# Kernel tuning notes

Measured on AMD Instinct MI355X. Metric: run time of the kernel, lower is better.

## Reference

```python
import jax, jax.numpy as jnp
import numpy as np

B, CIN, COUT, L, K, D = 64, 128, 256, 1024, 3, 2
P = (K - 1) * D  # causal padding = 4
THRESH = 0.1
SLOPE = 0.2  # LeakyReLU negative slope


def setup_inputs() -> dict:
    key = jax.random.key(0)
    ks = jax.random.split(key, 24)
    rn = lambda k, shape, s=0.05: jax.random.normal(k, shape, dtype=jnp.float32) * s
    return {
        "x": rn(ks[0], (B, CIN, L), 1.0),
        "conv1_w": rn(ks[1], (COUT, CIN, K)),
        "conv1_b": rn(ks[2], (COUT,)),
        "Wz_w": rn(ks[3], (COUT, COUT)), "Wz_b": rn(ks[4], (COUT,)),
        "Uz_w": rn(ks[5], (COUT, COUT)), "Uz_b": rn(ks[6], (COUT,)),
        "Wr_w": rn(ks[7], (COUT, COUT)), "Wr_b": rn(ks[8], (COUT,)),
        "Ur_w": rn(ks[9], (COUT, COUT)), "Ur_b": rn(ks[10], (COUT,)),
        "Wh_w": rn(ks[11], (COUT, COUT)), "Wh_b": rn(ks[12], (COUT,)),
        "Uh_w": rn(ks[13], (COUT, COUT)), "Uh_b": rn(ks[14], (COUT,)),
        "conv2_w": rn(ks[15], (COUT, COUT, K)),
        "conv2_b": rn(ks[16], (COUT,)),
        "skip_w": rn(ks[17], (COUT, CIN, 1)),
        "skip_b": rn(ks[18], (COUT,)),
        "aw": jnp.ones((1,), jnp.float32),  # AttentionZeroedLayer param, init ones
    }


def _causal_conv(x, w, b):
    # x: [B,C,L], w: [O,I,K]; pad both sides by P then chomp the right tail
    y = jax.lax.conv_general_dilated(
        x, w, window_strides=(1,), padding=[(P, P)], rhs_dilation=(D,),
        dimension_numbers=("NCH", "OIH", "NCH"))
    y = y + b[None, :, None]
    return y[:, :, :-P] if P > 0 else y


def reference(x, conv1_w, conv1_b, Wz_w, Wz_b, Uz_w, Uz_b, Wr_w, Wr_b,
              Ur_w, Ur_b, Wh_w, Wh_b, Uh_w, Uh_b, conv2_w, conv2_b,
              skip_w, skip_b, aw):
    res = x
    # conv1 -> chomp -> LeakyReLU (dropout=0, identity in eval)
    h1 = jax.nn.leaky_relu(_causal_conv(x, conv1_w, conv1_b), SLOPE)  # [B,COUT,L]
    xt = h1.transpose(0, 2, 1)  # [B,L,C]
    # precompute input-side GRU projections as batched GEMMs
    xz = jnp.einsum("blc,hc->blh", xt, Wz_w) + Wz_b
    xr = jnp.einsum("blc,hc->blh", xt, Wr_w) + Wr_b
    xh = jnp.einsum("blc,hc->blh", xt, Wh_w) + Wh_b

    def step(h, ins):
        xz_t, xr_t, xh_t = ins
        z = jax.nn.sigmoid(xz_t + h @ Uz_w.T + Uz_b)
        r = jax.nn.sigmoid(xr_t + h @ Ur_w.T + Ur_b)
        h_tilde = jnp.tanh(xh_t + r * (h @ Uh_w.T + Uh_b))
        h_new = (1 - z) * h + z * h_tilde
        return h_new, h_new

    h0 = jnp.zeros((B, COUT), x.dtype)
    _, hs = jax.lax.scan(step, h0, (xz.transpose(1, 0, 2),
                                    xr.transpose(1, 0, 2),
                                    xh.transpose(1, 0, 2)))  # [L,B,C]
    g = hs.transpose(1, 2, 0)  # [B,COUT,L]
    # AttentionZeroedLayer: zero elements with |g| < threshold * sigmoid(aw)
    gate = jax.nn.sigmoid(aw)[0]
    g = jnp.where(jnp.abs(g) < THRESH * gate, jnp.zeros_like(g), g)
    # conv2 -> chomp -> LeakyReLU
    y = jax.nn.leaky_relu(_causal_conv(g, conv2_w, conv2_b), SLOPE)
    # 1x1 skip connection (in_channels != out_channels)
    res = jax.lax.conv_general_dilated(
        res, skip_w, window_strides=(1,), padding=[(0, 0)],
        dimension_numbers=("NCH", "OIH", "NCH")) + skip_b[None, :, None]
    return y + res
```

## Files before the change

### kernel.cpp

```cpp
#include <hip/hip_runtime.h>
#include <hip/hip_bf16.h>


typedef _Float16 f16;
typedef _Float16 h2_t __attribute__((ext_vector_type(2)));

__device__ __forceinline__ float bf1(unsigned short s){ return __uint_as_float(((unsigned)s)<<16); }

__device__ __forceinline__ unsigned packh2(float a, float b){
  h2_t h; h[0] = (f16)a; h[1] = (f16)b;
  return *(unsigned*)&h;
}
__device__ __forceinline__ unsigned bf2h2(unsigned u){
  return packh2(bf1((unsigned short)(u & 0xffffu)), bf1((unsigned short)(u >> 16)));
}

__device__ __forceinline__ float fdot2(unsigned a, unsigned b, float c){
#if __has_builtin(__builtin_amdgcn_fdot2)
  return __builtin_amdgcn_fdot2(*(h2_t*)&a, *(h2_t*)&b, c, false);
#else
  h2_t x = *(h2_t*)&a, y = *(h2_t*)&b;
  return c + (float)x[0]*(float)y[0] + (float)x[1]*(float)y[1];
#endif
}

__device__ __forceinline__ unsigned short f2bf(float f){
  __hip_bfloat16 h = __float2bfloat16(f);
  return *(unsigned short*)&h;
}
__device__ __forceinline__ unsigned packbf2(float a, float b){
  return (unsigned)f2bf(a) | ((unsigned)f2bf(b)<<16);
}
__device__ __forceinline__ float h2lo(unsigned u){ h2_t h = *(h2_t*)&u; return (float)h[0]; }
__device__ __forceinline__ float h2hi(unsigned u){ h2_t h = *(h2_t*)&u; return (float)h[1]; }

__device__ __forceinline__ bool aw_is_f32(const void* aw){
  return ((const unsigned*)aw)[0] == 0x3F800000u;
}

__device__ __forceinline__ float dpp_add_b1(float v){
  int x = __builtin_amdgcn_update_dpp(0, __float_as_int(v), 0xB1, 0xF, 0xF, true);
  return v + __int_as_float(x);
}
__device__ __forceinline__ float dpp_add_4e(float v){
  int x = __builtin_amdgcn_update_dpp(0, __float_as_int(v), 0x4E, 0xF, 0xF, true);
  return v + __int_as_float(x);
}
__device__ __forceinline__ float red4(float v){
  return dpp_add_4e(dpp_add_b1(v));
}

__global__ void k_repack(const void* __restrict__ w1,  const void* __restrict__ w2,
                         const void* __restrict__ Wz,  const void* __restrict__ Wr,
                         const void* __restrict__ Wh,  const void* __restrict__ wsk,
                         const void* __restrict__ Uz,  const void* __restrict__ Ur,
                         const void* __restrict__ Uh,
                         const void* __restrict__ b1,  const void* __restrict__ Wzb,
                         const void* __restrict__ Wrb, const void* __restrict__ Whb,
                         const void* __restrict__ Uzb, const void* __restrict__ Urb,
                         const void* __restrict__ Uhb, const void* __restrict__ b2,
                         const void* __restrict__ bsk, const void* __restrict__ aw,
                         f16* __restrict__ p1, f16* __restrict__ p2,
                         f16* __restrict__ pz, f16* __restrict__ pr,
                         f16* __restrict__ ph, f16* __restrict__ ps,
                         f16* __restrict__ puz, f16* __restrict__ pur,
                         f16* __restrict__ puh, float* __restrict__ bc)
{
  const bool f32 = aw_is_f32(aw);
  auto G = [&](const void* p, int idx)->float{
    return f32 ? ((const float*)p)[idx] : bf1(((const unsigned short*)p)[idx]);
  };
  int i = blockIdx.x*256 + threadIdx.x;
  if (i < 196608){
    int t=i/65536, r=i%65536, cc=r>>11, r2=r&2047, o=r2>>3, ci=r2&7, c=cc*8+ci;
    p2[i] = (f16)G(w2, o*768 + c*3 + t);
  }
  if (i < 98304){
    int t=i/32768, r=i%32768, cc=r>>11, r2=r&2047, o=r2>>3, ci=r2&7, c=cc*8+ci;
    p1[i] = (f16)G(w1, o*384 + c*3 + t);
  }
  if (i < 65536){
    int cc=i>>11, r2=i&2047, o=r2>>3, ci=r2&7, c=cc*8+ci;
    int s = o*256 + c;
    pz[i]=(f16)G(Wz, s); pr[i]=(f16)G(Wr, s); ph[i]=(f16)G(Wh, s);
    puz[i]=(f16)G(Uz, i); pur[i]=(f16)G(Ur, i); puh[i]=(f16)G(Uh, i);
  }
  if (i < 32768){
    int cc=i>>11, r2=i&2047, o=r2>>3, ci=r2&7, c=cc*8+ci;
    ps[i]=(f16)G(wsk, o*128 + c);
  }
  if (i < 2304){
    int which = i>>8, j = i&255;
    const void* src[9] = {b1, Wzb, Wrb, Whb, Uzb, Urb, Uhb, b2, bsk};
    bc[i] = G(src[which], j);
  }
  if (i == 2304){
    float v = G(aw, 0);
    bc[2304] = 0.1f / (1.f + __expf(-v));
    bc[2305] = f32 ? 1.f : 0.f;
  }
}

__global__ __launch_bounds__(256,2) void k_conv1proj(
    const void* __restrict__ x,
    const f16* __restrict__ W1,
    const f16* __restrict__ WZ, const f16* __restrict__ WR, const f16* __restrict__ WH,
    const float* __restrict__ bc,
    f16* __restrict__ XZ, f16* __restrict__ XR, f16* __restrict__ XH,
    int Lc, int t0)
{
  __shared__ unsigned smem_u[12544];
  f16* xa = (f16*)smem_u;
  unsigned* tileA = smem_u + 4352;
  f16* hy = (f16*)(smem_u + 4352);
  const int b = blockIdx.y;
  const int lt = blockIdx.x*64;
  const int gl0 = t0 + lt;
  const int tid = threadIdx.x, lb = tid&7, ob = tid>>3;
  const bool f32 = (bc[2305] != 0.f);

  #pragma unroll
  for (int k=0;k<17;k++){
    int idx = tid + k*256;
    int c = idx/34, lp = idx - c*34;
    int gl = gl0 - 4 + lp*2;
    unsigned u = 0u;
    if (gl >= 0){
      if (f32){
        float2 v = *(const float2*)((const float*)x + ((size_t)b*128 + c)*1024 + gl);
        u = packh2(v.x, v.y);
      } else {
        u = bf2h2(*(const unsigned*)((const unsigned short*)x + ((size_t)b*128 + c)*1024 + gl));
      }
    }
    tileA[c*35 + lp] = u;
  }
  __syncthreads();
  #pragma unroll
  for (int k=0;k<17;k++){
    int idx = tid + k*256;
    int row = idx>>6, cp = idx&63;
    unsigned u0 = tileA[(2*cp)*35 + (row>>1)];
    unsigned u1 = tileA[(2*cp+1)*35 + (row>>1)];
    unsigned short s0 = (row&1)? (unsigned short)(u0>>16):(unsigned short)(u0&0xffffu);
    unsigned short s1 = (row&1)? (unsigned short)(u1>>16):(unsigned short)(u1&0xffffu);
    int sw = (cp>>2) ^ ((row>>3)&7);
    *(unsigned*)(&xa[row*128 + sw*8 + (cp&3)*2]) = (unsigned)s0 | ((unsigned)s1<<16);
  }
  __syncthreads();

  float acc[8][8];
  uint4 wreg[8], wnext[8];

  #pragma unroll
  for (int i=0;i<8;i++)
    #pragma unroll
    for (int j=0;j<8;j++) acc[i][j]=0.f;
  #pragma unroll
  for (int oi=0;oi<8;oi++) wreg[oi] = *(const uint4*)(W1 + ob*64 + oi*8);
  for (int ch=0; ch<48; ch++){
    if (ch+1 < 48){
      const f16* wn = W1 + (size_t)(ch+1)*2048 + ob*64;
      #pragma unroll
      for (int oi=0;oi<8;oi++) wnext[oi] = *(const uint4*)(wn + oi*8);
    }
    int t = ch>>4, cc = ch&15;
    #pragma unroll
    for (int li=0; li<8; li++){
      int row = lb*8 + li + t*2;
      int sw = cc ^ ((row>>3)&7);
      uint4 a = *(const uint4*)(&xa[row*128 + sw*8]);
      #pragma unroll
      for (int oi=0; oi<8; oi++){
        acc[li][oi] = fdot2(a.x, wreg[oi].x, acc[li][oi]);
        acc[li][oi] = fdot2(a.y, wreg[oi].y, acc[li][oi]);
        acc[li][oi] = fdot2(a.z, wreg[oi].z, acc[li][oi]);
        acc[li][oi] = fdot2(a.w, wreg[oi].w, acc[li][oi]);
      }
    }
    #pragma unroll
    for (int oi=0;oi<8;oi++) wreg[oi] = wnext[oi];
  }
  {
    const float* bp = bc + 0 + ob*8;
    #pragma unroll
    for (int li=0; li<8; li++){
      int row = lb*8 + li;
      f16 vals[8];
      #pragma unroll
      for (int oi=0;oi<8;oi++){
        float v = acc[li][oi] + bp[oi];
        vals[oi] = (f16)((v>0.f) ? v : 0.2f*v);
      }
      *(uint4*)(&hy[row*256 + ((ob ^ ((row>>3)&7))<<3)]) = *(uint4*)vals;
    }
  }
  __syncthreads();

  const f16* Wg[3] = {WZ, WR, WH};
  f16* Og[3] = {XZ, XR, XH};
  for (int g3=0; g3<3; g3++){
    const f16* Wp = Wg[g3];
    #pragma unroll
    for (int i=0;i<8;i++)
      #pragma unroll
      for (int j=0;j<8;j++) acc[i][j]=0.f;
    #pragma unroll
    for (int oi=0;oi<8;oi++) wreg[oi] = *(const uint4*)(Wp + ob*64 + oi*8);
    for (int ch=0; ch<32; ch++){
      if (ch+1 < 32){
        const f16* wn = Wp + (size_t)(ch+1)*2048 + ob*64;
        #pragma unroll
        for (int oi=0;oi<8;oi++) wnext[oi] = *(const uint4*)(wn + oi*8);
      }
      #pragma unroll
      for (int li=0; li<8; li++){
        int row = lb*8 + li;
        int sw = ch ^ ((row>>3)&7);
        uint4 a = *(const uint4*)(&hy[row*256 + sw*8]);
        #pragma unroll
        for (int oi=0; oi<8; oi++){
          acc[li][oi] = fdot2(a.x, wreg[oi].x, acc[li][oi]);
          acc[li][oi] = fdot2(a.y, wreg[oi].y, acc[li][oi]);
          acc[li][oi] = fdot2(a.z, wreg[oi].z, acc[li][oi]);
          acc[li][oi] = fdot2(a.w, wreg[oi].w, acc[li][oi]);
        }
      }
      #pragma unroll
      for (int oi=0;oi<8;oi++) wreg[oi] = wnext[oi];
    }
    f16* Ob = Og[g3] + ((size_t)b*Lc + lt)*256 + ob*8;
    #pragma unroll
    for (int li=0; li<8; li++){
      f16 vals[8];
      #pragma unroll
      for (int oi=0;oi<8;oi++){
        int o = ob*8 + oi;
        float bias = bc[256 + g3*256 + o] + ((g3<2) ? bc[1024 + g3*256 + o] : 0.f);
        vals[oi] = (f16)(acc[li][oi] + bias);
      }
      *(uint4*)(Ob + (size_t)(lb*8 + li)*256) = *(uint4*)vals;
    }
  }
}

__global__ __launch_bounds__(512, 1)
void k_scan(
    const f16* __restrict__ XZ, const f16* __restrict__ XR, const f16* __restrict__ XH,
    const f16* __restrict__ pUz, const f16* __restrict__ pUr, const f16* __restrict__ pUh,
    const float* __restrict__ bc,
    f16* __restrict__ G, float* __restrict__ carry,
    int Lc, int first)
{
  const int b = blockIdx.x, tid = threadIdx.x;
  const int kp = tid&3, grp = tid>>2, r0 = grp*2;
  __shared__ unsigned hb[2][160];

  {
    f16* gb = G + (size_t)b*(Lc+4)*256;
    int row = tid>>7, col = tid&127;
    unsigned v = 0u;
    if (!first) v = *(unsigned*)(gb + (size_t)(Lc+row)*256 + col*2);
    *(unsigned*)(gb + (size_t)row*256 + col*2) = v;
  }

  unsigned uz0[32],uz1[32],ur0[32],ur1[32],uh0[32],uh1[32];
  const int cbase = kp*64;
  #pragma unroll
  for (int j4=0;j4<8;j4++){
    uint4 q;
    q = *(const uint4*)(pUz + r0*256     + cbase + j4*8);
    uz0[j4*4+0]=q.x; uz0[j4*4+1]=q.y; uz0[j4*4+2]=q.z; uz0[j4*4+3]=q.w;
    q = *(const uint4*)(pUz + (r0+1)*256 + cbase + j4*8);
    uz1[j4*4+0]=q.x; uz1[j4*4+1]=q.y; uz1[j4*4+2]=q.z; uz1[j4*4+3]=q.w;
    q = *(const uint4*)(pUr + r0*256     + cbase + j4*8);
    ur0[j4*4+0]=q.x; ur0[j4*4+1]=q.y; ur0[j4*4+2]=q.z; ur0[j4*4+3]=q.w;
    q = *(const uint4*)(pUr + (r0+1)*256 + cbase + j4*8);
    ur1[j4*4+0]=q.x; ur1[j4*4+1]=q.y; ur1[j4*4+2]=q.z; ur1[j4*4+3]=q.w;
    q = *(const uint4*)(pUh + r0*256     + cbase + j4*8);
    uh0[j4*4+0]=q.x; uh0[j4*4+1]=q.y; uh0[j4*4+2]=q.z; uh0[j4*4+3]=q.w;
    q = *(const uint4*)(pUh + (r0+1)*256 + cbase + j4*8);
    uh1[j4*4+0]=q.x; uh1[j4*4+1]=q.y; uh1[j4*4+2]=q.z; uh1[j4*4+3]=q.w;
  }
  #pragma unroll
  for (int j=0;j<32;j++){
    asm volatile("" : "+v"(uz0[j]), "+v"(uz1[j]), "+v"(ur0[j]));
    asm volatile("" : "+v"(ur1[j]), "+v"(uh0[j]), "+v"(uh1[j]));
  }
  const float bh0=bc[1536+r0], bh1=bc[1536+r0+1];
  const float thr = bc[2304];
  float hp0, hp1;
  if (first){ hp0 = 0.f; hp1 = 0.f; }
  else { hp0 = carry[b*256 + r0]; hp1 = carry[b*256 + r0 + 1]; }
  const int wslot = (grp>>5)*40 + (grp&31);
  if (kp == 0) hb[0][wslot] = packh2(hp0, hp1);

  const f16* xzp = XZ + (size_t)b*Lc*256 + r0;
  const f16* xrp = XR + (size_t)b*Lc*256 + r0;
  const f16* xhp = XH + (size_t)b*Lc*256 + r0;
  f16* gp = G + (size_t)b*(Lc+4)*256 + r0;

  unsigned xzv = *(const unsigned*)(xzp);
  unsigned xrv = *(const unsigned*)(xrp);
  unsigned xhv = *(const unsigned*)(xhp);
  __syncthreads();

  for (int t=0; t<Lc; t++){
    const int tn = (t+1 < Lc) ? t+1 : t;
    const unsigned nz = *(const unsigned*)(xzp + (size_t)tn*256);
    const unsigned nr = *(const unsigned*)(xrp + (size_t)tn*256);
    const unsigned nh = *(const unsigned*)(xhp + (size_t)tn*256);

    const unsigned* hbr = hb[t&1] + kp*40;
    float az0=0,az1=0,ar0=0,ar1=0,ah0=0,ah1=0;
    #pragma unroll
    for (int j4=0;j4<8;j4++){
      const uint4 hv = *(const uint4*)(hbr + j4*4);
      const unsigned hw[4] = {hv.x, hv.y, hv.z, hv.w};
      #pragma unroll
      for (int p=0;p<4;p++){
        const int J = j4*4+p;
        az0 = fdot2(hw[p], uz0[J], az0);
        az1 = fdot2(hw[p], uz1[J], az1);
        ar0 = fdot2(hw[p], ur0[J], ar0);
        ar1 = fdot2(hw[p], ur1[J], ar1);
        ah0 = fdot2(hw[p], uh0[J], ah0);
        ah1 = fdot2(hw[p], uh1[J], ah1);
      }
    }
    az0 = red4(az0); az1 = red4(az1);
    ar0 = red4(ar0); ar1 = red4(ar1);
    ah0 = red4(ah0); ah1 = red4(ah1);

    const float z0  = 1.f/(1.f+__expf(-(h2lo(xzv)+az0)));
    const float z1  = 1.f/(1.f+__expf(-(h2hi(xzv)+az1)));
    const float rr0 = 1.f/(1.f+__expf(-(h2lo(xrv)+ar0)));
    const float rr1 = 1.f/(1.f+__expf(-(h2hi(xrv)+ar1)));
    const float e0  = __expf(2.f*(h2lo(xhv)+rr0*(ah0+bh0)));
    const float e1  = __expf(2.f*(h2hi(xhv)+rr1*(ah1+bh1)));
    const float hh0 = 1.f - 2.f/(e0+1.f);
    const float hh1 = 1.f - 2.f/(e1+1.f);
    const float hn0 = (1.f-z0)*hp0 + z0*hh0;
    const float hn1 = (1.f-z1)*hp1 + z1*hh1;
    hp0 = hn0; hp1 = hn1;
    if (kp == 0){
      const float g0 = (fabsf(hn0) < thr) ? 0.f : hn0;
      const float g1 = (fabsf(hn1) < thr) ? 0.f : hn1;
      *(unsigned*)(gp + (size_t)(t+4)*256) = packh2(g0, g1);
      hb[(t+1)&1][wslot] = packh2(hn0, hn1);
    }
    xzv = nz; xrv = nr; xhv = nh;
    __syncthreads();
  }
  if (kp == 0){
    carry[b*256 + r0]     = hp0;
    carry[b*256 + r0 + 1] = hp1;
  }
}

__global__ __launch_bounds__(256,2) void k_final(const f16* __restrict__ G,
    const void* __restrict__ x, const f16* __restrict__ W2,
    const f16* __restrict__ WS, const float* __restrict__ bc,
    void* __restrict__ out, int Lc, int t0)
{
  __shared__ unsigned smem2[8704];
  f16* atG = (f16*)smem2;
  const int b = blockIdx.y;
  const int lt = blockIdx.x*64;
  const int gl0 = t0 + lt;
  const int tid = threadIdx.x, lb = tid&7, ob = tid>>3;
  const bool f32 = (bc[2305] != 0.f);

  {
    const f16* Ab = G + (size_t)b*(Lc+4)*256 + (size_t)lt*256;
    for (int idx=tid; idx<68*32; idx+=256){
      int row = idx>>5, cc = idx&31;
      uint4 v = *(const uint4*)(Ab + (size_t)row*256 + cc*8);
      *(uint4*)(&atG[row*256 + ((cc ^ ((row>>3)&7))<<3)]) = v;
    }
  }
  __syncthreads();

  float acc[8][8];
  #pragma unroll
  for (int i=0;i<8;i++)
    #pragma unroll
    for (int j=0;j<8;j++) acc[i][j]=0.f;

  uint4 wreg[8], wnext[8];
  #pragma unroll
  for (int oi=0;oi<8;oi++) wreg[oi] = *(const uint4*)(W2 + ob*64 + oi*8);
  for (int ch=0; ch<96; ch++){
    if (ch+1 < 96){
      const f16* wn = W2 + (size_t)(ch+1)*2048 + ob*64;
      #pragma unroll
      for (int oi=0;oi<8;oi++) wnext[oi] = *(const uint4*)(wn + oi*8);
    }
    int t = ch>>5, cc = ch&31;
    #pragma unroll
    for (int li=0; li<8; li++){
      int row = lb*8 + li + t*2;
      uint4 a = *(const uint4*)(&atG[row*256 + ((cc ^ ((row>>3)&7))<<3)]);
      #pragma unroll
      for (int oi=0; oi<8; oi++){
        acc[li][oi] = fdot2(a.x, wreg[oi].x, acc[li][oi]);
        acc[li][oi] = fdot2(a.y, wreg[oi].y, acc[li][oi]);
        acc[li][oi] = fdot2(a.z, wreg[oi].z, acc[li][oi]);
        acc[li][oi] = fdot2(a.w, wreg[oi].w, acc[li][oi]);
      }
    }
    #pragma unroll
    for (int oi=0;oi<8;oi++) wreg[oi] = wnext[oi];
  }
  {
    const float* bp = bc + 1792 + ob*8;
    #pragma unroll
    for (int li=0;li<8;li++)
      #pragma unroll
      for (int oi=0;oi<8;oi++){
        float v = acc[li][oi] + bp[oi];
        acc[li][oi] = (v>0.f) ? v : 0.2f*v;
      }
  }
  __syncthreads();

  unsigned* tileB = smem2;
  f16* xa2 = (f16*)(smem2 + 4352);
  #pragma unroll
  for (int k=0;k<16;k++){
    int idx = tid + k*256;
    int c = idx>>5, lp = idx&31;
    unsigned u;
    if (f32){
      float2 v = *(const float2*)((const float*)x + ((size_t)b*128 + c)*1024 + gl0 + lp*2);
      u = packh2(v.x, v.y);
    } else {
      u = bf2h2(*(const unsigned*)((const unsigned short*)x + ((size_t)b*128 + c)*1024 + gl0 + lp*2));
    }
    tileB[c*33 + lp] = u;
  }
  __syncthreads();
  #pragma unroll
  for (int k=0;k<16;k++){
    int idx = tid + k*256;
    int row = idx>>6, cp = idx&63;
    unsigned u0 = tileB[(2*cp)*33 + (row>>1)];
    unsigned u1 = tileB[(2*cp+1)*33 + (row>>1)];
    unsigned short s0 = (row&1)? (unsigned short)(u0>>16):(unsigned short)(u0&0xffffu);
    unsigned short s1 = (row&1)? (unsigned short)(u1>>16):(unsigned short)(u1&0xffffu);
    int sw = (cp>>2) ^ ((row>>3)&7);
    *(unsigned*)(&xa2[row*128 + sw*8 + (cp&3)*2]) = (unsigned)s0 | ((unsigned)s1<<16);
  }
  __syncthreads();

  #pragma unroll
  for (int oi=0;oi<8;oi++) wreg[oi] = *(const uint4*)(WS + ob*64 + oi*8);
  for (int ch=0; ch<16; ch++){
    if (ch+1 < 16){
      const f16* wn = WS + (size_t)(ch+1)*2048 + ob*64;
      #pragma unroll
      for (int oi=0;oi<8;oi++) wnext[oi] = *(const uint4*)(wn + oi*8);
    }
    #pragma unroll
    for (int li=0; li<8; li++){
      int row = lb*8 + li;
      int sw = ch ^ ((row>>3)&7);
      uint4 a = *(const uint4*)(&xa2[row*128 + sw*8]);
      #pragma unroll
      for (int oi=0; oi<8; oi++){
        acc[li][oi] = fdot2(a.x, wreg[oi].x, acc[li][oi]);
        acc[li][oi] = fdot2(a.y, wreg[oi].y, acc[li][oi]);
        acc[li][oi] = fdot2(a.z, wreg[oi].z, acc[li][oi]);
        acc[li][oi] = fdot2(a.w, wreg[oi].w, acc[li][oi]);
      }
    }
    #pragma unroll
    for (int oi=0;oi<8;oi++) wreg[oi] = wnext[oi];
  }
  {
    const float* sp = bc + 2048 + ob*8;
    #pragma unroll
    for (int oi=0;oi<8;oi++){
      int o = ob*8 + oi;
      size_t base = ((size_t)b*256 + o)*1024 + gl0 + lb*8;
      if (f32){
        float st[8];
        #pragma unroll
        for (int j=0;j<8;j++) st[j] = acc[j][oi] + sp[oi];
        *(uint4*)((float*)out + base)     = *(uint4*)&st[0];
        *(uint4*)((float*)out + base + 4) = *(uint4*)&st[4];
      } else {
        unsigned st[4];
        #pragma unroll
        for (int j=0;j<4;j++)
          st[j] = packbf2(acc[2*j][oi] + sp[oi], acc[2*j+1][oi] + sp[oi]);
        *(uint4*)((unsigned short*)out + base) = *(uint4*)st;
      }
    }
  }
}

extern "C" void kernel_launch(void* const* d_in, const int* in_sizes, int n_in,
                              void* d_out, int out_size, void* d_ws, size_t ws_size,
                              hipStream_t stream)
{
  const void* x   = d_in[0];
  const void* w1  = d_in[1];
  const void* b1  = d_in[2];
  const void* Wz  = d_in[3];
  const void* Wzb = d_in[4];
  const void* Uz  = d_in[5];
  const void* Uzb = d_in[6];
  const void* Wr  = d_in[7];
  const void* Wrb = d_in[8];
  const void* Ur  = d_in[9];
  const void* Urb = d_in[10];
  const void* Wh  = d_in[11];
  const void* Whb = d_in[12];
  const void* Uh  = d_in[13];
  const void* Uhb = d_in[14];
  const void* w2  = d_in[15];
  const void* b2  = d_in[16];
  const void* wsk = d_in[17];
  const void* bsk = d_in[18];
  const void* aw  = d_in[19];

  auto need = [](long long Lc)->size_t{
    return (size_t)(2LL*(758784LL + 3LL*64*Lc*256 + 64LL*(Lc+4)*256));
  };
  int Lc = 1024;
  if (ws_size < need(1024)) Lc = 256;
  if (ws_size < need(256))  Lc = 64;
  const int NCH = 1024 / Lc;

  f16* W = (f16*)d_ws;
  f16*   w1p   = W;
  f16*   w2p   = W + 98304;
  f16*   wzp   = W + 294912;
  f16*   wrp   = W + 360448;
  f16*   whp   = W + 425984;
  f16*   wsp   = W + 491520;
  f16*   uzp   = W + 524288;
  f16*   urp   = W + 589824;
  f16*   uhp   = W + 655360;
  float* bc    = (float*)(W + 720896);
  float* carry = (float*)(W + 726016);
  f16*   xz    = W + 758784;
  f16*   xr    = xz + (size_t)64*Lc*256;
  f16*   xh    = xr + (size_t)64*Lc*256;
  f16*   g     = xh + (size_t)64*Lc*256;

  k_repack<<<dim3(768), 256, 0, stream>>>(w1, w2, Wz, Wr, Wh, wsk, Uz, Ur, Uh,
                                          b1, Wzb, Wrb, Whb, Uzb, Urb, Uhb, b2,
                                          bsk, aw,
                                          w1p, w2p, wzp, wrp, whp, wsp,
                                          uzp, urp, uhp, bc);
  for (int c = 0; c < NCH; c++){
    const int t0 = c * Lc;
    const int first = (c == 0) ? 1 : 0;
    k_conv1proj<<<dim3(Lc/64,64), 256, 0, stream>>>(x, w1p, wzp, wrp, whp, bc,
                                                    xz, xr, xh, Lc, t0);
    k_scan<<<dim3(64), 512, 0, stream>>>(xz, xr, xh, uzp, urp, uhp, bc,
                                         g, carry, Lc, first);
    k_final<<<dim3(Lc/64,64), 256, 0, stream>>>(g, x, w2p, wsp, bc,
                                                d_out, Lc, t0);
  }
}
```

Baseline: 2.242 ms.

## Split GRU scan dot products across eight lanes with 1024-thread blocks

The recurrent scan kernel now gives each pair of hidden rows to 8 lanes instead of 4, and launches 1024 threads per batch block. This halves each thread's serial fdot2 chain and its per-thread U-weight register footprint. The lane reduction gains a ds_swizzle xor-4 step, and the hidden-state shared buffer layout is adjusted to match. The explicit next-timestep prefetch of the gate inputs is removed, so those global loads are issued each step. In exchange, every step's barrier now spans twice as many waves and the reduction adds latency.

```diff
diff --git a/kernel.cpp b/kernel.cpp
--- a/kernel.cpp
+++ b/kernel.cpp
@@ -46,8 +46,10 @@
   int x = __builtin_amdgcn_update_dpp(0, __float_as_int(v), 0x4E, 0xF, 0xF, true);
   return v + __int_as_float(x);
 }
-__device__ __forceinline__ float red4(float v){
-  return dpp_add_4e(dpp_add_b1(v));
+__device__ __forceinline__ float red8(float v){
+  v = dpp_add_4e(dpp_add_b1(v));
+  int x = __builtin_amdgcn_ds_swizzle(__float_as_int(v), 0x101F);
+  return v + __int_as_float(x);
 }
 
 __global__ void k_repack(const void* __restrict__ w1,  const void* __restrict__ w2,
@@ -244,7 +246,7 @@
   }
 }
 
-__global__ __launch_bounds__(512, 1)
+__global__ __launch_bounds__(1024)
 void k_scan(
     const f16* __restrict__ XZ, const f16* __restrict__ XR, const f16* __restrict__ XH,
     const f16* __restrict__ pUz, const f16* __restrict__ pUr, const f16* __restrict__ pUh,
@@ -253,10 +255,10 @@
     int Lc, int first)
 {
   const int b = blockIdx.x, tid = threadIdx.x;
-  const int kp = tid&3, grp = tid>>2, r0 = grp*2;
+  const int kp = tid&7, grp = tid>>3, r0 = grp*2;
   __shared__ unsigned hb[2][160];
 
-  {
+  if (tid < 512){
     f16* gb = G + (size_t)b*(Lc+4)*256;
     int row = tid>>7, col = tid&127;
     unsigned v = 0u;
@@ -264,10 +266,10 @@
     *(unsigned*)(gb + (size_t)row*256 + col*2) = v;
   }
 
-  unsigned uz0[32],uz1[32],ur0[32],ur1[32],uh0[32],uh1[32];
-  const int cbase = kp*64;
-  #pragma unroll
-  for (int j4=0;j4<8;j4++){
+  unsigned uz0[16],uz1[16],ur0[16],ur1[16],uh0[16],uh1[16];
+  const int cbase = kp*32;
+  #pragma unroll
+  for (int j4=0;j4<4;j4++){
     uint4 q;
     q = *(const uint4*)(pUz + r0*256     + cbase + j4*8);
     uz0[j4*4+0]=q.x; uz0[j4*4+1]=q.y; uz0[j4*4+2]=q.z; uz0[j4*4+3]=q.w;
@@ -283,38 +285,33 @@
     uh1[j4*4+0]=q.x; uh1[j4*4+1]=q.y; uh1[j4*4+2]=q.z; uh1[j4*4+3]=q.w;
   }
   #pragma unroll
-  for (int j=0;j<32;j++){
-    asm volatile("" : "+v"(uz0[j]), "+v"(uz1[j]), "+v"(ur0[j]));
-    asm volatile("" : "+v"(ur1[j]), "+v"(uh0[j]), "+v"(uh1[j]));
+  for (int j=0;j<16;j++){
+    asm volatile("" : "+v"(uz0[j]), "+v"(uz1[j]), "+v"(ur0[j]),
+                     "+v"(ur1[j]), "+v"(uh0[j]), "+v"(uh1[j]));
   }
   const float bh0=bc[1536+r0], bh1=bc[1536+r0+1];
   const float thr = bc[2304];
   float hp0, hp1;
   if (first){ hp0 = 0.f; hp1 = 0.f; }
   else { hp0 = carry[b*256 + r0]; hp1 = carry[b*256 + r0 + 1]; }
-  const int wslot = (grp>>5)*40 + (grp&31);
+  const int wslot = (grp>>4)*20 + (grp&15);
   if (kp == 0) hb[0][wslot] = packh2(hp0, hp1);
 
   const f16* xzp = XZ + (size_t)b*Lc*256 + r0;
   const f16* xrp = XR + (size_t)b*Lc*256 + r0;
   const f16* xhp = XH + (size_t)b*Lc*256 + r0;
   f16* gp = G + (size_t)b*(Lc+4)*256 + r0;
-
-  unsigned xzv = *(const unsigned*)(xzp);
-  unsigned xrv = *(const unsigned*)(xrp);
-  unsigned xhv = *(const unsigned*)(xhp);
   __syncthreads();
 
   for (int t=0; t<Lc; t++){
-    const int tn = (t+1 < Lc) ? t+1 : t;
-    const unsigned nz = *(const unsigned*)(xzp + (size_t)tn*256);
-    const unsigned nr = *(const unsigned*)(xrp + (size_t)tn*256);
-    const unsigned nh = *(const unsigned*)(xhp + (size_t)tn*256);
-
-    const unsigned* hbr = hb[t&1] + kp*40;
+    const unsigned xzv = *(const unsigned*)(xzp + (size_t)t*256);
+    const unsigned xrv = *(const unsigned*)(xrp + (size_t)t*256);
+    const unsigned xhv = *(const unsigned*)(xhp + (size_t)t*256);
+
+    const unsigned* hbr = hb[t&1] + kp*20;
     float az0=0,az1=0,ar0=0,ar1=0,ah0=0,ah1=0;
     #pragma unroll
-    for (int j4=0;j4<8;j4++){
+    for (int j4=0;j4<4;j4++){
       const uint4 hv = *(const uint4*)(hbr + j4*4);
       const unsigned hw[4] = {hv.x, hv.y, hv.z, hv.w};
       #pragma unroll
@@ -328,9 +325,9 @@
         ah1 = fdot2(hw[p], uh1[J], ah1);
       }
     }
-    az0 = red4(az0); az1 = red4(az1);
-    ar0 = red4(ar0); ar1 = red4(ar1);
-    ah0 = red4(ah0); ah1 = red4(ah1);
+    az0 = red8(az0); az1 = red8(az1);
+    ar0 = red8(ar0); ar1 = red8(ar1);
+    ah0 = red8(ah0); ah1 = red8(ah1);
 
     const float z0  = 1.f/(1.f+__expf(-(h2lo(xzv)+az0)));
     const float z1  = 1.f/(1.f+__expf(-(h2hi(xzv)+az1)));
@@ -349,7 +346,6 @@
       *(unsigned*)(gp + (size_t)(t+4)*256) = packh2(g0, g1);
       hb[(t+1)&1][wslot] = packh2(hn0, hn1);
     }
-    xzv = nz; xrv = nr; xhv = nh;
     __syncthreads();
   }
   if (kp == 0){
@@ -560,8 +556,8 @@
     const int first = (c == 0) ? 1 : 0;
     k_conv1proj<<<dim3(Lc/64,64), 256, 0, stream>>>(x, w1p, wzp, wrp, whp, bc,
                                                     xz, xr, xh, Lc, t0);
-    k_scan<<<dim3(64), 512, 0, stream>>>(xz, xr, xh, uzp, urp, uhp, bc,
-                                         g, carry, Lc, first);
+    k_scan<<<dim3(64), 1024, 0, stream>>>(xz, xr, xh, uzp, urp, uhp, bc,
+                                          g, carry, Lc, first);
     k_final<<<dim3(Lc/64,64), 256, 0, stream>>>(g, x, w2p, wsp, bc,
                                                 d_out, Lc, t0);
   }
```

New measurement: 3.075 ms. +37.2%, slower.
